# Performance work log

Measured on AMD Instinct MI355X. Metric: run time of the kernel, lower is better.

The kernel has to match this reference:

```python
import jax, jax.numpy as jnp
import numpy as np

D, H, B, NSTEPS = 128, 512, 128, 16


def setup_inputs() -> dict:
    key = jax.random.key(0)
    k0, k1, k2, k3 = jax.random.split(key, 4)
    s1 = 1.0 / np.sqrt(D)
    s2 = 0.1 / np.sqrt(H)  # small output scale keeps the flow well-conditioned
    return {
        "x0": jax.random.normal(k0, (B, D), jnp.float32),
        "W1": jax.random.normal(k1, (D, H), jnp.float32) * s1,
        "b1": jnp.zeros((H,), jnp.float32),
        "u1": jax.random.normal(k2, (H,), jnp.float32) * 0.1,
        "W2": jax.random.normal(k3, (H, D), jnp.float32) * s2,
        "b2": jnp.zeros((D,), jnp.float32),
        "n_steps": NSTEPS,
    }


def reference(x0, W1, b1, u1, W2, b2, n_steps):
    d = x0.shape[-1]
    LOG2PI = float(np.log(2.0 * np.pi))
    # log prob of x0 under standard-normal prior p0
    log_px0 = -0.5 * jnp.sum(x0 * x0, axis=-1) - 0.5 * d * LOG2PI
    dt = 1.0 / n_steps

    sg = jax.lax.stop_gradient
    W1s, b1s, u1s, W2s, b2s = sg(W1), sg(b1), sg(u1), sg(W2), sg(b2)

    def vf(t, x, w1, c1, v1, w2, c2):  # time-conditioned MLP vector field, x: (d,)
        return jnp.tanh(x @ w1 + c1 + t * v1) @ w2 + c2

    eye = jnp.eye(d, dtype=x0.dtype)

    def f_single(t, x):
        # exact Jacobian trace via vmapped JVP over identity tangents (stop-grad params)
        apply_sg = lambda xx: vf(t, xx, W1s, b1s, u1s, W2s, b2s)
        jvp1 = lambda e: jax.jvp(apply_sg, (x,), (e,))[1]
        jac = jax.vmap(jvp1)(eye)              # (d, d)
        dxdt = vf(t, x, W1, b1, u1, W2, b2)    # with grad-carrying params
        dlogpxdt = -jnp.trace(jac)
        gradlogpx = -x                          # grad log of standard-normal target
        dkldt = -jnp.vdot(gradlogpx, dxdt) + dlogpxdt
        return dxdt, dlogpxdt, dkldt

    rhs = jax.vmap(f_single, in_axes=(None, 0))  # batch over samples

    # Dopri5 Butcher tableau (fixed-step 5th-order solution)
    A = (
        (1 / 5,),
        (3 / 40, 9 / 40),
        (44 / 45, -56 / 15, 32 / 9),
        (19372 / 6561, -25360 / 2187, 64448 / 6561, -212 / 729),
        (9017 / 3168, -355 / 33, 46732 / 5247, 49 / 176, -5103 / 18656),
    )
    C = (1 / 5, 3 / 10, 4 / 5, 8 / 9, 1.0)
    BW = (35 / 384, 0.0, 500 / 1113, 125 / 192, -2187 / 6784, 11 / 84)

    def lin(y, ks, cs):  # y + dt * sum(c_i * k_i), tree-structured state
        return jax.tree_util.tree_map(
            lambda yv, *kv: yv + dt * sum(c * k for c, k in zip(cs, kv)), y, *ks)

    def step(y, t):
        ks = [rhs(t, y[0])]
        for ai, ci in zip(A, C):
            yi = lin(y, ks, ai)
            ks.append(rhs(t + ci * dt, yi[0]))
        return lin(y, ks, BW), None

    nb = x0.shape[0]
    y0 = (x0, jnp.zeros((nb,), x0.dtype), jnp.zeros((nb,), x0.dtype))
    ts = jnp.arange(n_steps, dtype=x0.dtype) * dt
    (z, log_det, kl), _ = jax.lax.scan(step, y0, ts)
    log_px = log_px0 + log_det
    return z, log_px, kl
```

## Files before the change

kernel.cpp:

```cpp
#include <hip/hip_runtime.h>

#define TPB 1024

typedef _Float16 hf2 __attribute__((ext_vector_type(2)));

__device__ __forceinline__ hf2 as_h2(unsigned u) { return __builtin_bit_cast(hf2, u); }
__device__ __forceinline__ unsigned pk2h(float a, float b) {
    unsigned la = (unsigned)__builtin_bit_cast(unsigned short, (_Float16)a);
    unsigned hb = (unsigned)__builtin_bit_cast(unsigned short, (_Float16)b);
    return la | (hb << 16);
}
#define FDOT2(w, x, acc) __builtin_amdgcn_fdot2(as_h2(w), as_h2(x), (acc), false)

#define DPPADD(v, CTRL) ((v) + __int_as_float(__builtin_amdgcn_update_dpp( \
    0, __float_as_int(v), (CTRL), 0xF, 0xF, false)))
#define SWZADD(v, OFF) ((v) + __int_as_float(__builtin_amdgcn_ds_swizzle( \
    __float_as_int(v), (OFF))))
#define RED4(v)  { v = DPPADD(v, 0xB1); v = DPPADD(v, 0x4E); }
#define RED16(v) { v = DPPADD(v, 0xB1); v = DPPADD(v, 0x4E); \
                   v = SWZADD(v, 0x101F); v = DPPADD(v, 0x128); }

#define RED64(v) { v += __shfl_xor(v,32,64); v += __shfl_xor(v,16,64); \
  v += __shfl_xor(v,8,64); v += __shfl_xor(v,4,64); v += __shfl_xor(v,2,64); \
  v += __shfl_xor(v,1,64); }

#define G4(M) M(0) M(1) M(2) M(3)

__global__ __launch_bounds__(TPB, 1) void vi_node_kernel(
    const float* __restrict__ x0, const float* __restrict__ W1,
    const float* __restrict__ b1, const float* __restrict__ u1,
    const float* __restrict__ W2, const float* __restrict__ b2,
    const int* __restrict__ nsp, float* __restrict__ out, int nB)
{
    const int s  = blockIdx.x;
    const int t  = threadIdx.x;
    const int l  = t & 63;
    const int w  = t >> 6;
    const int rg    = l & 3;
    const int cpair = 16 * w + (l >> 2);
    const int c0 = 2 * cpair, c1 = c0 + 1;
    const int rg4   = l & 15;
    const int jpair = 4 * w + (l >> 4);
    const int j0 = 2 * jpair, j1 = j0 + 1;

    __shared__ __align__(16) unsigned xsPK[64];
    __shared__ __align__(16) unsigned aPKp[320];
    __shared__ float redA[16], redB[16], sqred[2];

#define DECLW(cc) unsigned wA##cc##_0, wA##cc##_1, wA##cc##_2, wA##cc##_3, \
                           wB##cc##_0, wB##cc##_1, wB##cc##_2, wB##cc##_3; \
                  unsigned zA##cc##_0, zA##cc##_1, zA##cc##_2, zA##cc##_3, \
                           zB##cc##_0, zB##cc##_1, zB##cc##_2, zB##cc##_3;
    G4(DECLW)

#define LDW1(cc) { const int r_ = 32 * rg + 8 * (cc); \
    wA##cc##_0 = pk2h(W1[(r_+0)*512+c0], W1[(r_+1)*512+c0]); \
    wA##cc##_1 = pk2h(W1[(r_+2)*512+c0], W1[(r_+3)*512+c0]); \
    wA##cc##_2 = pk2h(W1[(r_+4)*512+c0], W1[(r_+5)*512+c0]); \
    wA##cc##_3 = pk2h(W1[(r_+6)*512+c0], W1[(r_+7)*512+c0]); \
    wB##cc##_0 = pk2h(W1[(r_+0)*512+c1], W1[(r_+1)*512+c1]); \
    wB##cc##_1 = pk2h(W1[(r_+2)*512+c1], W1[(r_+3)*512+c1]); \
    wB##cc##_2 = pk2h(W1[(r_+4)*512+c1], W1[(r_+5)*512+c1]); \
    wB##cc##_3 = pk2h(W1[(r_+6)*512+c1], W1[(r_+7)*512+c1]); }
    G4(LDW1)

#define LDW2(cc) { const int r_ = 32 * rg4 + 8 * (cc); \
    zA##cc##_0 = pk2h(W2[(r_+0)*128+j0], W2[(r_+1)*128+j0]); \
    zA##cc##_1 = pk2h(W2[(r_+2)*128+j0], W2[(r_+3)*128+j0]); \
    zA##cc##_2 = pk2h(W2[(r_+4)*128+j0], W2[(r_+5)*128+j0]); \
    zA##cc##_3 = pk2h(W2[(r_+6)*128+j0], W2[(r_+7)*128+j0]); \
    zB##cc##_0 = pk2h(W2[(r_+0)*128+j1], W2[(r_+1)*128+j1]); \
    zB##cc##_1 = pk2h(W2[(r_+2)*128+j1], W2[(r_+3)*128+j1]); \
    zB##cc##_2 = pk2h(W2[(r_+4)*128+j1], W2[(r_+5)*128+j1]); \
    zB##cc##_3 = pk2h(W2[(r_+6)*128+j1], W2[(r_+7)*128+j1]); }
    G4(LDW2)

    float wd0 = 0.f, wd1 = 0.f;
#pragma unroll
    for (int i = 0; i < 32; ++i) {
        const int r_ = 32 * rg + i;
        wd0 = fmaf(W1[r_ * 512 + c0], W2[c0 * 128 + r_], wd0);
        wd1 = fmaf(W1[r_ * 512 + c1], W2[c1 * 128 + r_], wd1);
    }
    RED4(wd0) RED4(wd1)

    const float b1k0 = b1[c0], b1k1 = b1[c1];
    const float u1k0 = u1[c0], u1k1 = u1[c1];
    const float b2j0 = b2[j0], b2j1 = b2[j1];

    const int ns = nsp[0];
    const float dt = 1.f / (float)ns;

    if (t < 64) xsPK[t] = pk2h(x0[s * 128 + 2 * t], x0[s * 128 + 2 * t + 1]);
    if (t < 128) {
        float xv = x0[s * 128 + t];
        float sq = xv * xv;
        RED64(sq)
        if (l == 0) sqred[w] = sq;
    }
    float xc0 = x0[s * 128 + j0], xc1 = x0[s * 128 + j1];
    float yc0 = xc0, yc1 = xc1;
    float k0_0=0.f,k0_1=0.f,k1_0=0.f,k1_1=0.f,k2_0=0.f,k2_1=0.f,
          k3_0=0.f,k3_1=0.f,k4_0=0.f,k4_1=0.f;
    float tr_loc = 0.f, dot_loc = 0.f;
    __syncthreads();

#define HM(cc) { const uint4 xq = *(const uint4*)&xsPK[16 * rg + 4 * (cc)]; \
    a0 = FDOT2(wA##cc##_0, xq.x, a0); a1 = FDOT2(wA##cc##_1, xq.y, a1); \
    a0 = FDOT2(wA##cc##_2, xq.z, a0); a1 = FDOT2(wA##cc##_3, xq.w, a1); \
    b0 = FDOT2(wB##cc##_0, xq.x, b0); b1v = FDOT2(wB##cc##_1, xq.y, b1v); \
    b0 = FDOT2(wB##cc##_2, xq.z, b0); b1v = FDOT2(wB##cc##_3, xq.w, b1v); }

#define PM(cc) { const uint4 aq = *(const uint4*)&aPKp[20 * rg4 + 4 * (cc)]; \
    p0 = FDOT2(zA##cc##_0, aq.x, p0); p1 = FDOT2(zA##cc##_1, aq.y, p1); \
    p0 = FDOT2(zA##cc##_2, aq.z, p0); p1 = FDOT2(zA##cc##_3, aq.w, p1); \
    q0 = FDOT2(zB##cc##_0, aq.x, q0); q1 = FDOT2(zB##cc##_1, aq.y, q1); \
    q0 = FDOT2(zB##cc##_2, aq.z, q0); q1 = FDOT2(zB##cc##_3, aq.w, q1); }

#define EVAL(CW, TVAL, KST0, KST1, XN0, XN1, LAST)                             \
    {                                                                          \
        float a0=0.f, a1=0.f, b0=0.f, b1v=0.f;                                 \
        HM(0) HM(1) HM(2) HM(3)                                                \
        float sA = a0 + a1, sB = b0 + b1v;                                     \
        RED4(sA) RED4(sB)                           \
        float h0 = fmaf((TVAL), u1k0, b1k0) + sA;                              \
        float h1 = fmaf((TVAL), u1k1, b1k1) + sB;                              \
        float aa0 = 1.f - 2.f / (__expf(2.f * h0) + 1.f);                      \
        float aa1 = 1.f - 2.f / (__expf(2.f * h1) + 1.f);                      \
        if (rg == 0)                                                           \
            aPKp[(cpair >> 4) * 20 + (cpair & 15)] = pk2h(aa0, aa1);           \
        tr_loc = fmaf((CW), fmaf(-aa0, aa0, 1.f) * wd0                         \
                          + fmaf(-aa1, aa1, 1.f) * wd1, tr_loc);               \
        __syncthreads();                                   \
        float p0=0.f, p1=0.f, q0=0.f, q1=0.f;                                  \
        PM(0) PM(1) PM(2) PM(3)                                                \
        float sp = p0 + p1, sq_ = q0 + q1;                                     \
        RED16(sp) RED16(sq_)                      \
        float dx0 = sp + b2j0, dx1 = sq_ + b2j1;                               \
        dot_loc = fmaf((CW), xc0 * dx0 + xc1 * dx1, dot_loc);                  \
        KST0; KST1;                                                            \
        xc0 = (XN0); xc1 = (XN1);                                              \
        if (LAST) { yc0 = xc0; yc1 = xc1; }                                    \
        if ((l & 15) == 0) xsPK[jpair] = pk2h(xc0, xc1);                       \
        __syncthreads();                                   \
    }

    for (int n = 0; n < ns; ++n) {
        const float tn = (float)n;

        EVAL((float)(35.0/384.0), tn * dt, k0_0 = dx0, k0_1 = dx1,
             fmaf(dt, 0.2f * dx0, yc0), fmaf(dt, 0.2f * dx1, yc1), 0)

        EVAL(0.0f, (tn + 0.2f) * dt, k1_0 = dx0, k1_1 = dx1,
             yc0 + dt * (0.075f * k0_0 + 0.225f * dx0),
             yc1 + dt * (0.075f * k0_1 + 0.225f * dx1), 0)

        EVAL((float)(500.0/1113.0), (tn + 0.3f) * dt, k2_0 = dx0, k2_1 = dx1,
             yc0 + dt * ((float)(44.0/45.0) * k0_0 + (float)(-56.0/15.0) * k1_0
                       + (float)(32.0/9.0)  * dx0),
             yc1 + dt * ((float)(44.0/45.0) * k0_1 + (float)(-56.0/15.0) * k1_1
                       + (float)(32.0/9.0)  * dx1), 0)

        EVAL((float)(125.0/192.0), (tn + 0.8f) * dt, k3_0 = dx0, k3_1 = dx1,
             yc0 + dt * ((float)(19372.0/6561.0) * k0_0 + (float)(-25360.0/2187.0) * k1_0
                       + (float)(64448.0/6561.0) * k2_0 + (float)(-212.0/729.0)    * dx0),
             yc1 + dt * ((float)(19372.0/6561.0) * k0_1 + (float)(-25360.0/2187.0) * k1_1
                       + (float)(64448.0/6561.0) * k2_1 + (float)(-212.0/729.0)    * dx1), 0)

        EVAL((float)(-2187.0/6784.0), (tn + (float)(8.0/9.0)) * dt, k4_0 = dx0, k4_1 = dx1,
             yc0 + dt * ((float)(9017.0/3168.0)  * k0_0 + (float)(-355.0/33.0) * k1_0
                       + (float)(46732.0/5247.0) * k2_0 + (float)(49.0/176.0)  * k3_0
                       + (float)(-5103.0/18656.0) * dx0),
             yc1 + dt * ((float)(9017.0/3168.0)  * k0_1 + (float)(-355.0/33.0) * k1_1
                       + (float)(46732.0/5247.0) * k2_1 + (float)(49.0/176.0)  * k3_1
                       + (float)(-5103.0/18656.0) * dx1), 0)

        EVAL((float)(11.0/84.0), (tn + 1.0f) * dt, (void)0, (void)0,
             yc0 + dt * ((float)(35.0/384.0)  * k0_0 + (float)(500.0/1113.0)   * k2_0
                       + (float)(125.0/192.0) * k3_0 + (float)(-2187.0/6784.0) * k4_0
                       + (float)(11.0/84.0)   * dx0),
             yc1 + dt * ((float)(35.0/384.0)  * k0_1 + (float)(500.0/1113.0)   * k2_1
                       + (float)(125.0/192.0) * k3_1 + (float)(-2187.0/6784.0) * k4_1
                       + (float)(11.0/84.0)   * dx1), 1)
    }

    {
        float tv = tr_loc;  RED64(tv)  if (l == 0) redA[w] = tv;
        float dv = dot_loc; RED64(dv)  if (l == 0) redB[w] = dv;
    }
    __syncthreads();

    if ((l & 15) == 0) {
        out[s * 128 + j0] = yc0;
        out[s * 128 + j1] = yc1;
    }
    if (t == 0) {
        float TRs = 0.f, DOs = 0.f;
#pragma unroll
        for (int ww = 0; ww < 16; ++ww) { TRs += redA[ww]; DOs += redB[ww]; }
        const float TR = TRs * dt * 0.25f;
        const float DO = DOs * dt * (1.f / 16.f);
        const float LOG2PI = 1.8378770664093454f;
        float lpx0 = -0.5f * (sqred[0] + sqred[1]) - 0.5f * 128.f * LOG2PI;
        out[nB * 128 + s]      = lpx0 - TR;
        out[nB * 128 + nB + s] = DO - TR;
    }
}

extern "C" void kernel_launch(void* const* d_in, const int* in_sizes, int n_in,
                              void* d_out, int out_size, void* d_ws, size_t ws_size,
                              hipStream_t stream) {
    const float* x0 = (const float*)d_in[0];
    const float* W1 = (const float*)d_in[1];
    const float* b1 = (const float*)d_in[2];
    const float* u1 = (const float*)d_in[3];
    const float* W2 = (const float*)d_in[4];
    const float* b2 = (const float*)d_in[5];
    const int*  nsp = (const int*)d_in[6];
    float* out = (float*)d_out;
    const int nB = in_sizes[0] / 128;

    hipLaunchKernelGGL(vi_node_kernel, dim3(nB), dim3(TPB), 0, stream,
                       x0, W1, b1, u1, W2, b2, nsp, out, nB);
}
```

Baseline: 262.6 us.

## Halve block size, give each thread four outputs, stage W2 in swizzled LDS

Cuts the block from 1024 to 512 threads, so each thread owns four hidden columns and four output dims instead of two. W1 is staged through shared memory as packed fp16 for coalesced loading, then held in registers, while W2 now stays in a 128KB XOR-swizzled shared-memory array and is read each evaluation. Only rg==0 lanes compute tanh, the RED16 swizzle is replaced by DPP, and RK stage values are kept in packed fp16 to save registers. This gives more work per thread and fewer waves at each barrier, at the cost of extra LDS traffic for W2 and fp16 rounding of the intermediate k values.

```diff
diff --git a/kernel.cpp b/kernel.cpp
--- a/kernel.cpp
+++ b/kernel.cpp
@@ -1,6 +1,6 @@
 #include <hip/hip_runtime.h>
 
-#define TPB 1024
+#define TPB 512
 
 typedef _Float16 hf2 __attribute__((ext_vector_type(2)));
 
@@ -11,20 +11,20 @@
     return la | (hb << 16);
 }
 #define FDOT2(w, x, acc) __builtin_amdgcn_fdot2(as_h2(w), as_h2(x), (acc), false)
+#define UPa(u) ((float)(as_h2(u).x))
+#define UPb(u) ((float)(as_h2(u).y))
 
 #define DPPADD(v, CTRL) ((v) + __int_as_float(__builtin_amdgcn_update_dpp( \
     0, __float_as_int(v), (CTRL), 0xF, 0xF, false)))
-#define SWZADD(v, OFF) ((v) + __int_as_float(__builtin_amdgcn_ds_swizzle( \
-    __float_as_int(v), (OFF))))
 #define RED4(v)  { v = DPPADD(v, 0xB1); v = DPPADD(v, 0x4E); }
 #define RED16(v) { v = DPPADD(v, 0xB1); v = DPPADD(v, 0x4E); \
-                   v = SWZADD(v, 0x101F); v = DPPADD(v, 0x128); }
-
+                   v = DPPADD(v, 0x124); v = DPPADD(v, 0x128); }
 #define RED64(v) { v += __shfl_xor(v,32,64); v += __shfl_xor(v,16,64); \
   v += __shfl_xor(v,8,64); v += __shfl_xor(v,4,64); v += __shfl_xor(v,2,64); \
   v += __shfl_xor(v,1,64); }
 
-#define G4(M) M(0) M(1) M(2) M(3)
+#define G16(M) M(0) M(1) M(2) M(3) M(4) M(5) M(6) M(7) M(8) M(9) M(10) M(11) \
+  M(12) M(13) M(14) M(15)
 
 __global__ __launch_bounds__(TPB, 1) void vi_node_kernel(
     const float* __restrict__ x0, const float* __restrict__ W1,
@@ -36,61 +36,45 @@
     const int t  = threadIdx.x;
     const int l  = t & 63;
     const int w  = t >> 6;
-    const int rg    = l & 3;
-    const int cpair = 16 * w + (l >> 2);
-    const int c0 = 2 * cpair, c1 = c0 + 1;
-    const int rg4   = l & 15;
-    const int jpair = 4 * w + (l >> 4);
-    const int j0 = 2 * jpair, j1 = j0 + 1;
-
+    const int rg  = t & 3;
+    const int cg  = t >> 2;
+    const int rg4 = t & 15;
+    const int jg  = t >> 4;
+
+    __shared__ __align__(16) unsigned BIG[32768];
     __shared__ __align__(16) unsigned xsPK[64];
     __shared__ __align__(16) unsigned aPKp[320];
-    __shared__ float redA[16], redB[16], sqred[2];
-
-#define DECLW(cc) unsigned wA##cc##_0, wA##cc##_1, wA##cc##_2, wA##cc##_3, \
-                           wB##cc##_0, wB##cc##_1, wB##cc##_2, wB##cc##_3; \
-                  unsigned zA##cc##_0, zA##cc##_1, zA##cc##_2, zA##cc##_3, \
-                           zB##cc##_0, zB##cc##_1, zB##cc##_2, zB##cc##_3;
-    G4(DECLW)
-
-#define LDW1(cc) { const int r_ = 32 * rg + 8 * (cc); \
-    wA##cc##_0 = pk2h(W1[(r_+0)*512+c0], W1[(r_+1)*512+c0]); \
-    wA##cc##_1 = pk2h(W1[(r_+2)*512+c0], W1[(r_+3)*512+c0]); \
-    wA##cc##_2 = pk2h(W1[(r_+4)*512+c0], W1[(r_+5)*512+c0]); \
-    wA##cc##_3 = pk2h(W1[(r_+6)*512+c0], W1[(r_+7)*512+c0]); \
-    wB##cc##_0 = pk2h(W1[(r_+0)*512+c1], W1[(r_+1)*512+c1]); \
-    wB##cc##_1 = pk2h(W1[(r_+2)*512+c1], W1[(r_+3)*512+c1]); \
-    wB##cc##_2 = pk2h(W1[(r_+4)*512+c1], W1[(r_+5)*512+c1]); \
-    wB##cc##_3 = pk2h(W1[(r_+6)*512+c1], W1[(r_+7)*512+c1]); }
-    G4(LDW1)
-
-#define LDW2(cc) { const int r_ = 32 * rg4 + 8 * (cc); \
-    zA##cc##_0 = pk2h(W2[(r_+0)*128+j0], W2[(r_+1)*128+j0]); \
-    zA##cc##_1 = pk2h(W2[(r_+2)*128+j0], W2[(r_+3)*128+j0]); \
-    zA##cc##_2 = pk2h(W2[(r_+4)*128+j0], W2[(r_+5)*128+j0]); \
-    zA##cc##_3 = pk2h(W2[(r_+6)*128+j0], W2[(r_+7)*128+j0]); \
-    zB##cc##_0 = pk2h(W2[(r_+0)*128+j1], W2[(r_+1)*128+j1]); \
-    zB##cc##_1 = pk2h(W2[(r_+2)*128+j1], W2[(r_+3)*128+j1]); \
-    zB##cc##_2 = pk2h(W2[(r_+4)*128+j1], W2[(r_+5)*128+j1]); \
-    zB##cc##_3 = pk2h(W2[(r_+6)*128+j1], W2[(r_+7)*128+j1]); }
-    G4(LDW2)
-
-    float wd0 = 0.f, wd1 = 0.f;
-#pragma unroll
-    for (int i = 0; i < 32; ++i) {
-        const int r_ = 32 * rg + i;
-        wd0 = fmaf(W1[r_ * 512 + c0], W2[c0 * 128 + r_], wd0);
-        wd1 = fmaf(W1[r_ * 512 + c1], W2[c1 * 128 + r_], wd1);
-    }
-    RED4(wd0) RED4(wd1)
-
-    const float b1k0 = b1[c0], b1k1 = b1[c1];
-    const float u1k0 = u1[c0], u1k1 = u1[c1];
-    const float b2j0 = b2[j0], b2j1 = b2[j1];
-
-    const int ns = nsp[0];
-    const float dt = 1.f / (float)ns;
-
+    __shared__ float redA[8], redB[8], sqred[2];
+
+    for (int idx = t; idx < 32768; idx += TPB) {
+        const int rp = idx >> 9, col = idx & 511;
+        BIG[(rp << 9) + col] =
+            pk2h(W1[(2 * rp) * 512 + col], W1[(2 * rp + 1) * 512 + col]);
+    }
+    __syncthreads();
+
+#define DECLW1(i) unsigned w1_##i##_0, w1_##i##_1, w1_##i##_2, w1_##i##_3;
+    G16(DECLW1)
+#define LDW1(i) { const uint4 v_ = *(const uint4*)&BIG[((16*rg + (i)) << 9) + 4*cg]; \
+    w1_##i##_0 = v_.x; w1_##i##_1 = v_.y; w1_##i##_2 = v_.z; w1_##i##_3 = v_.w; }
+    G16(LDW1)
+
+    float wd0 = 0.f, wd1 = 0.f, wd2 = 0.f, wd3 = 0.f;
+#define WDI(i) { const int r2_ = 2 * (16 * rg + (i)); \
+    wd0 = FDOT2(w1_##i##_0, pk2h(W2[(4*cg+0)*128 + r2_], W2[(4*cg+0)*128 + r2_ + 1]), wd0); \
+    wd1 = FDOT2(w1_##i##_1, pk2h(W2[(4*cg+1)*128 + r2_], W2[(4*cg+1)*128 + r2_ + 1]), wd1); \
+    wd2 = FDOT2(w1_##i##_2, pk2h(W2[(4*cg+2)*128 + r2_], W2[(4*cg+2)*128 + r2_ + 1]), wd2); \
+    wd3 = FDOT2(w1_##i##_3, pk2h(W2[(4*cg+3)*128 + r2_], W2[(4*cg+3)*128 + r2_ + 1]), wd3); }
+    G16(WDI)
+    RED4(wd0) RED4(wd1) RED4(wd2) RED4(wd3)
+
+    __syncthreads();
+
+    for (int idx = t; idx < 32768; idx += TPB) {
+        const int rp = idx >> 7, c = idx & 127;
+        BIG[(rp << 7) + (c ^ (((rp >> 4) & 7) << 2))] =
+            pk2h(W2[(2 * rp) * 128 + c], W2[(2 * rp + 1) * 128 + c]);
+    }
     if (t < 64) xsPK[t] = pk2h(x0[s * 128 + 2 * t], x0[s * 128 + 2 * t + 1]);
     if (t < 128) {
         float xv = x0[s * 128 + t];
@@ -98,90 +82,151 @@
         RED64(sq)
         if (l == 0) sqred[w] = sq;
     }
-    float xc0 = x0[s * 128 + j0], xc1 = x0[s * 128 + j1];
-    float yc0 = xc0, yc1 = xc1;
-    float k0_0=0.f,k0_1=0.f,k1_0=0.f,k1_1=0.f,k2_0=0.f,k2_1=0.f,
-          k3_0=0.f,k3_1=0.f,k4_0=0.f,k4_1=0.f;
+
+    const unsigned b1p_a = pk2h(b1[4*cg+0], b1[4*cg+1]);
+    const unsigned b1p_b = pk2h(b1[4*cg+2], b1[4*cg+3]);
+    const unsigned u1p_a = pk2h(u1[4*cg+0], u1[4*cg+1]);
+    const unsigned u1p_b = pk2h(u1[4*cg+2], u1[4*cg+3]);
+    const unsigned b2p_a = pk2h(b2[4*jg+0], b2[4*jg+1]);
+    const unsigned b2p_b = pk2h(b2[4*jg+2], b2[4*jg+3]);
+
+    float xc0 = x0[s*128 + 4*jg+0], xc1 = x0[s*128 + 4*jg+1];
+    float xc2 = x0[s*128 + 4*jg+2], xc3 = x0[s*128 + 4*jg+3];
+    float yc0 = xc0, yc1 = xc1, yc2 = xc2, yc3 = xc3;
+    unsigned k0a=0,k0b=0,k1a=0,k1b=0,k2a=0,k2b=0,k3a=0,k3b=0,k4a=0,k4b=0;
     float tr_loc = 0.f, dot_loc = 0.f;
-    __syncthreads();
-
-#define HM(cc) { const uint4 xq = *(const uint4*)&xsPK[16 * rg + 4 * (cc)]; \
-    a0 = FDOT2(wA##cc##_0, xq.x, a0); a1 = FDOT2(wA##cc##_1, xq.y, a1); \
-    a0 = FDOT2(wA##cc##_2, xq.z, a0); a1 = FDOT2(wA##cc##_3, xq.w, a1); \
-    b0 = FDOT2(wB##cc##_0, xq.x, b0); b1v = FDOT2(wB##cc##_1, xq.y, b1v); \
-    b0 = FDOT2(wB##cc##_2, xq.z, b0); b1v = FDOT2(wB##cc##_3, xq.w, b1v); }
-
-#define PM(cc) { const uint4 aq = *(const uint4*)&aPKp[20 * rg4 + 4 * (cc)]; \
-    p0 = FDOT2(zA##cc##_0, aq.x, p0); p1 = FDOT2(zA##cc##_1, aq.y, p1); \
-    p0 = FDOT2(zA##cc##_2, aq.z, p0); p1 = FDOT2(zA##cc##_3, aq.w, p1); \
-    q0 = FDOT2(zB##cc##_0, aq.x, q0); q1 = FDOT2(zB##cc##_1, aq.y, q1); \
-    q0 = FDOT2(zB##cc##_2, aq.z, q0); q1 = FDOT2(zB##cc##_3, aq.w, q1); }
-
-#define EVAL(CW, TVAL, KST0, KST1, XN0, XN1, LAST)                             \
+
+    const int ns = nsp[0];
+    const float dt = 1.f / (float)ns;
+
+    const int xoff  = 16 * rg;
+    const int aoff  = 20 * rg4;
+    const int w2off = (rg4 << 11) + ((jg ^ (rg4 & 7)) << 2);
+    const int apk_w = (cg >> 3) * 20 + ((2 * cg) & 15);
+    const int xs_w  = 2 * jg;
+
+    __syncthreads();
+
+#define HM(cc, i0, i1, i2, i3) { const uint4 xq = *(const uint4*)&xsPK[xoff + 4*(cc)]; \
+    a0  = FDOT2(w1_##i0##_0, xq.x, a0);  a1f = FDOT2(w1_##i0##_1, xq.x, a1f); \
+    a2  = FDOT2(w1_##i0##_2, xq.x, a2);  a3  = FDOT2(w1_##i0##_3, xq.x, a3); \
+    a0  = FDOT2(w1_##i1##_0, xq.y, a0);  a1f = FDOT2(w1_##i1##_1, xq.y, a1f); \
+    a2  = FDOT2(w1_##i1##_2, xq.y, a2);  a3  = FDOT2(w1_##i1##_3, xq.y, a3); \
+    a0  = FDOT2(w1_##i2##_0, xq.z, a0);  a1f = FDOT2(w1_##i2##_1, xq.z, a1f); \
+    a2  = FDOT2(w1_##i2##_2, xq.z, a2);  a3  = FDOT2(w1_##i2##_3, xq.z, a3); \
+    a0  = FDOT2(w1_##i3##_0, xq.w, a0);  a1f = FDOT2(w1_##i3##_1, xq.w, a1f); \
+    a2  = FDOT2(w1_##i3##_2, xq.w, a2);  a3  = FDOT2(w1_##i3##_3, xq.w, a3); }
+
+#define PMJ(cc, j, AE) { const uint4 wq = *(const uint4*)&BIG[w2off + ((4*(cc)+(j)) << 7)]; \
+    p0 = FDOT2(wq.x, AE, p0); p1 = FDOT2(wq.y, AE, p1); \
+    p2 = FDOT2(wq.z, AE, p2); p3 = FDOT2(wq.w, AE, p3); }
+#define PM(cc) { const uint4 aq = *(const uint4*)&aPKp[aoff + 4*(cc)]; \
+    PMJ(cc,0,aq.x) PMJ(cc,1,aq.y) PMJ(cc,2,aq.z) PMJ(cc,3,aq.w) }
+
+#define EVAL(CW, TVAL, KST, XN0, XN1, XN2, XN3, LAST)                          \
     {                                                                          \
-        float a0=0.f, a1=0.f, b0=0.f, b1v=0.f;                                 \
-        HM(0) HM(1) HM(2) HM(3)                                                \
-        float sA = a0 + a1, sB = b0 + b1v;                                     \
-        RED4(sA) RED4(sB)                           \
-        float h0 = fmaf((TVAL), u1k0, b1k0) + sA;                              \
-        float h1 = fmaf((TVAL), u1k1, b1k1) + sB;                              \
-        float aa0 = 1.f - 2.f / (__expf(2.f * h0) + 1.f);                      \
-        float aa1 = 1.f - 2.f / (__expf(2.f * h1) + 1.f);                      \
-        if (rg == 0)                                                           \
-            aPKp[(cpair >> 4) * 20 + (cpair & 15)] = pk2h(aa0, aa1);           \
-        tr_loc = fmaf((CW), fmaf(-aa0, aa0, 1.f) * wd0                         \
-                          + fmaf(-aa1, aa1, 1.f) * wd1, tr_loc);               \
+        float a0 = 0.f, a1f = 0.f, a2 = 0.f, a3 = 0.f;                         \
+        HM(0, 0,1,2,3) HM(1, 4,5,6,7) HM(2, 8,9,10,11) HM(3, 12,13,14,15)      \
+        RED4(a0) RED4(a1f) RED4(a2) RED4(a3)                                   \
+        if (rg == 0) {                                                         \
+            const float tv_ = (TVAL);                                          \
+            float h0 = fmaf(tv_, UPa(u1p_a), UPa(b1p_a)) + a0;                 \
+            float h1 = fmaf(tv_, UPb(u1p_a), UPb(b1p_a)) + a1f;                \
+            float h2 = fmaf(tv_, UPa(u1p_b), UPa(b1p_b)) + a2;                 \
+            float h3 = fmaf(tv_, UPb(u1p_b), UPb(b1p_b)) + a3;                 \
+            float t0 = 1.f - 2.f / (__expf(2.f * h0) + 1.f);                   \
+            float t1 = 1.f - 2.f / (__expf(2.f * h1) + 1.f);                   \
+            float t2 = 1.f - 2.f / (__expf(2.f * h2) + 1.f);                   \
+            float t3 = 1.f - 2.f / (__expf(2.f * h3) + 1.f);                   \
+            *(uint2*)&aPKp[apk_w] = make_uint2(pk2h(t0, t1), pk2h(t2, t3));    \
+            tr_loc = fmaf((CW), fmaf(-t0, t0, 1.f) * wd0                       \
+                               + fmaf(-t1, t1, 1.f) * wd1                      \
+                               + fmaf(-t2, t2, 1.f) * wd2                      \
+                               + fmaf(-t3, t3, 1.f) * wd3, tr_loc);            \
+        }                                                                      \
         __syncthreads();                                   \
-        float p0=0.f, p1=0.f, q0=0.f, q1=0.f;                                  \
+        float p0 = 0.f, p1 = 0.f, p2 = 0.f, p3 = 0.f;                          \
         PM(0) PM(1) PM(2) PM(3)                                                \
-        float sp = p0 + p1, sq_ = q0 + q1;                                     \
-        RED16(sp) RED16(sq_)                      \
-        float dx0 = sp + b2j0, dx1 = sq_ + b2j1;                               \
-        dot_loc = fmaf((CW), xc0 * dx0 + xc1 * dx1, dot_loc);                  \
-        KST0; KST1;                                                            \
-        xc0 = (XN0); xc1 = (XN1);                                              \
-        if (LAST) { yc0 = xc0; yc1 = xc1; }                                    \
-        if ((l & 15) == 0) xsPK[jpair] = pk2h(xc0, xc1);                       \
+        RED16(p0) RED16(p1) RED16(p2) RED16(p3)                                \
+        float dx0 = p0 + UPa(b2p_a), dx1 = p1 + UPb(b2p_a);                    \
+        float dx2 = p2 + UPa(b2p_b), dx3 = p3 + UPb(b2p_b);                    \
+        dot_loc = fmaf((CW), xc0*dx0 + xc1*dx1 + xc2*dx2 + xc3*dx3, dot_loc);  \
+        KST;                                                                   \
+        float K00 = UPa(k0a), K01 = UPb(k0a), K02 = UPa(k0b), K03 = UPb(k0b);  \
+        float K10 = UPa(k1a), K11 = UPb(k1a), K12 = UPa(k1b), K13 = UPb(k1b);  \
+        float K20 = UPa(k2a), K21 = UPb(k2a), K22 = UPa(k2b), K23 = UPb(k2b);  \
+        float K30 = UPa(k3a), K31 = UPb(k3a), K32 = UPa(k3b), K33 = UPb(k3b);  \
+        float K40 = UPa(k4a), K41 = UPb(k4a), K42 = UPa(k4b), K43 = UPb(k4b);  \
+        (void)K00;(void)K01;(void)K02;(void)K03;(void)K10;(void)K11;(void)K12; \
+        (void)K13;(void)K20;(void)K21;(void)K22;(void)K23;(void)K30;(void)K31; \
+        (void)K32;(void)K33;(void)K40;(void)K41;(void)K42;(void)K43;           \
+        float xn0 = (XN0), xn1 = (XN1), xn2 = (XN2), xn3 = (XN3);              \
+        xc0 = xn0; xc1 = xn1; xc2 = xn2; xc3 = xn3;                            \
+        if (LAST) { yc0 = xn0; yc1 = xn1; yc2 = xn2; yc3 = xn3; }              \
+        if ((l & 15) == 0)                                                     \
+            *(uint2*)&xsPK[xs_w] = make_uint2(pk2h(xn0, xn1), pk2h(xn2, xn3)); \
         __syncthreads();                                   \
     }
 
     for (int n = 0; n < ns; ++n) {
         const float tn = (float)n;
 
-        EVAL((float)(35.0/384.0), tn * dt, k0_0 = dx0, k0_1 = dx1,
-             fmaf(dt, 0.2f * dx0, yc0), fmaf(dt, 0.2f * dx1, yc1), 0)
-
-        EVAL(0.0f, (tn + 0.2f) * dt, k1_0 = dx0, k1_1 = dx1,
-             yc0 + dt * (0.075f * k0_0 + 0.225f * dx0),
-             yc1 + dt * (0.075f * k0_1 + 0.225f * dx1), 0)
-
-        EVAL((float)(500.0/1113.0), (tn + 0.3f) * dt, k2_0 = dx0, k2_1 = dx1,
-             yc0 + dt * ((float)(44.0/45.0) * k0_0 + (float)(-56.0/15.0) * k1_0
-                       + (float)(32.0/9.0)  * dx0),
-             yc1 + dt * ((float)(44.0/45.0) * k0_1 + (float)(-56.0/15.0) * k1_1
-                       + (float)(32.0/9.0)  * dx1), 0)
-
-        EVAL((float)(125.0/192.0), (tn + 0.8f) * dt, k3_0 = dx0, k3_1 = dx1,
-             yc0 + dt * ((float)(19372.0/6561.0) * k0_0 + (float)(-25360.0/2187.0) * k1_0
-                       + (float)(64448.0/6561.0) * k2_0 + (float)(-212.0/729.0)    * dx0),
-             yc1 + dt * ((float)(19372.0/6561.0) * k0_1 + (float)(-25360.0/2187.0) * k1_1
-                       + (float)(64448.0/6561.0) * k2_1 + (float)(-212.0/729.0)    * dx1), 0)
-
-        EVAL((float)(-2187.0/6784.0), (tn + (float)(8.0/9.0)) * dt, k4_0 = dx0, k4_1 = dx1,
-             yc0 + dt * ((float)(9017.0/3168.0)  * k0_0 + (float)(-355.0/33.0) * k1_0
-                       + (float)(46732.0/5247.0) * k2_0 + (float)(49.0/176.0)  * k3_0
-                       + (float)(-5103.0/18656.0) * dx0),
-             yc1 + dt * ((float)(9017.0/3168.0)  * k0_1 + (float)(-355.0/33.0) * k1_1
-                       + (float)(46732.0/5247.0) * k2_1 + (float)(49.0/176.0)  * k3_1
-                       + (float)(-5103.0/18656.0) * dx1), 0)
-
-        EVAL((float)(11.0/84.0), (tn + 1.0f) * dt, (void)0, (void)0,
-             yc0 + dt * ((float)(35.0/384.0)  * k0_0 + (float)(500.0/1113.0)   * k2_0
-                       + (float)(125.0/192.0) * k3_0 + (float)(-2187.0/6784.0) * k4_0
-                       + (float)(11.0/84.0)   * dx0),
-             yc1 + dt * ((float)(35.0/384.0)  * k0_1 + (float)(500.0/1113.0)   * k2_1
-                       + (float)(125.0/192.0) * k3_1 + (float)(-2187.0/6784.0) * k4_1
-                       + (float)(11.0/84.0)   * dx1), 1)
+        EVAL((float)(35.0/384.0), tn * dt,
+             (k0a = pk2h(dx0,dx1), k0b = pk2h(dx2,dx3)),
+             fmaf(dt, 0.2f*dx0, yc0), fmaf(dt, 0.2f*dx1, yc1),
+             fmaf(dt, 0.2f*dx2, yc2), fmaf(dt, 0.2f*dx3, yc3), 0)
+
+        EVAL(0.0f, (tn + 0.2f) * dt,
+             (k1a = pk2h(dx0,dx1), k1b = pk2h(dx2,dx3)),
+             yc0 + dt*(0.075f*K00 + 0.225f*dx0), yc1 + dt*(0.075f*K01 + 0.225f*dx1),
+             yc2 + dt*(0.075f*K02 + 0.225f*dx2), yc3 + dt*(0.075f*K03 + 0.225f*dx3), 0)
+
+        EVAL((float)(500.0/1113.0), (tn + 0.3f) * dt,
+             (k2a = pk2h(dx0,dx1), k2b = pk2h(dx2,dx3)),
+             yc0 + dt*((float)(44.0/45.0)*K00 + (float)(-56.0/15.0)*K10 + (float)(32.0/9.0)*dx0),
+             yc1 + dt*((float)(44.0/45.0)*K01 + (float)(-56.0/15.0)*K11 + (float)(32.0/9.0)*dx1),
+             yc2 + dt*((float)(44.0/45.0)*K02 + (float)(-56.0/15.0)*K12 + (float)(32.0/9.0)*dx2),
+             yc3 + dt*((float)(44.0/45.0)*K03 + (float)(-56.0/15.0)*K13 + (float)(32.0/9.0)*dx3), 0)
+
+        EVAL((float)(125.0/192.0), (tn + 0.8f) * dt,
+             (k3a = pk2h(dx0,dx1), k3b = pk2h(dx2,dx3)),
+             yc0 + dt*((float)(19372.0/6561.0)*K00 + (float)(-25360.0/2187.0)*K10
+                     + (float)(64448.0/6561.0)*K20 + (float)(-212.0/729.0)*dx0),
+             yc1 + dt*((float)(19372.0/6561.0)*K01 + (float)(-25360.0/2187.0)*K11
+                     + (float)(64448.0/6561.0)*K21 + (float)(-212.0/729.0)*dx1),
+             yc2 + dt*((float)(19372.0/6561.0)*K02 + (float)(-25360.0/2187.0)*K12
+                     + (float)(64448.0/6561.0)*K22 + (float)(-212.0/729.0)*dx2),
+             yc3 + dt*((float)(19372.0/6561.0)*K03 + (float)(-25360.0/2187.0)*K13
+                     + (float)(64448.0/6561.0)*K23 + (float)(-212.0/729.0)*dx3), 0)
+
+        EVAL((float)(-2187.0/6784.0), (tn + (float)(8.0/9.0)) * dt,
+             (k4a = pk2h(dx0,dx1), k4b = pk2h(dx2,dx3)),
+             yc0 + dt*((float)(9017.0/3168.0)*K00 + (float)(-355.0/33.0)*K10
+                     + (float)(46732.0/5247.0)*K20 + (float)(49.0/176.0)*K30
+                     + (float)(-5103.0/18656.0)*dx0),
+             yc1 + dt*((float)(9017.0/3168.0)*K01 + (float)(-355.0/33.0)*K11
+                     + (float)(46732.0/5247.0)*K21 + (float)(49.0/176.0)*K31
+                     + (float)(-5103.0/18656.0)*dx1),
+             yc2 + dt*((float)(9017.0/3168.0)*K02 + (float)(-355.0/33.0)*K12
+                     + (float)(46732.0/5247.0)*K22 + (float)(49.0/176.0)*K32
+                     + (float)(-5103.0/18656.0)*dx2),
+             yc3 + dt*((float)(9017.0/3168.0)*K03 + (float)(-355.0/33.0)*K13
+                     + (float)(46732.0/5247.0)*K23 + (float)(49.0/176.0)*K33
+                     + (float)(-5103.0/18656.0)*dx3), 0)
+
+        EVAL((float)(11.0/84.0), (tn + 1.0f) * dt, (void)0,
+             yc0 + dt*((float)(35.0/384.0)*K00 + (float)(500.0/1113.0)*K20
+                     + (float)(125.0/192.0)*K30 + (float)(-2187.0/6784.0)*K40
+                     + (float)(11.0/84.0)*dx0),
+             yc1 + dt*((float)(35.0/384.0)*K01 + (float)(500.0/1113.0)*K21
+                     + (float)(125.0/192.0)*K31 + (float)(-2187.0/6784.0)*K41
+                     + (float)(11.0/84.0)*dx1),
+             yc2 + dt*((float)(35.0/384.0)*K02 + (float)(500.0/1113.0)*K22
+                     + (float)(125.0/192.0)*K32 + (float)(-2187.0/6784.0)*K42
+                     + (float)(11.0/84.0)*dx2),
+             yc3 + dt*((float)(35.0/384.0)*K03 + (float)(500.0/1113.0)*K23
+                     + (float)(125.0/192.0)*K33 + (float)(-2187.0/6784.0)*K43
+                     + (float)(11.0/84.0)*dx3), 1)
     }
 
     {
@@ -191,14 +236,16 @@
     __syncthreads();
 
     if ((l & 15) == 0) {
-        out[s * 128 + j0] = yc0;
-        out[s * 128 + j1] = yc1;
+        out[s * 128 + 4*jg + 0] = yc0;
+        out[s * 128 + 4*jg + 1] = yc1;
+        out[s * 128 + 4*jg + 2] = yc2;
+        out[s * 128 + 4*jg + 3] = yc3;
     }
     if (t == 0) {
         float TRs = 0.f, DOs = 0.f;
 #pragma unroll
-        for (int ww = 0; ww < 16; ++ww) { TRs += redA[ww]; DOs += redB[ww]; }
-        const float TR = TRs * dt * 0.25f;
+        for (int ww = 0; ww < 8; ++ww) { TRs += redA[ww]; DOs += redB[ww]; }
+        const float TR = TRs * dt;
         const float DO = DOs * dt * (1.f / 16.f);
         const float LOG2PI = 1.8378770664093454f;
         float lpx0 = -0.5f * (sqred[0] + sqred[1]) - 0.5f * 128.f * LOG2PI;
```

Measured after the change: 226.3 us. 13.8% less time.
